# Kernel optimization log

Measured on AMD Instinct MI355X. Metric: run time of the kernel, lower is better.

Reference implementation:

```python
import jax, jax.numpy as jnp
import numpy as np

MU, SIGMA = -9.1232, 3.5412
FFT_SIZES = [8, 16, 32, 64]
HOP_SIZES = [2, 4, 8, 16]
EPS_MAG, EPS_SC = 1e-7, 1e-8


def hann_periodic(n):
    # torch.hann_window default (periodic=True)
    return 0.5 * (1.0 - jnp.cos(2.0 * jnp.pi * jnp.arange(n, dtype=jnp.float32) / n))


def stft_mag(xf, n_fft, hop):
    # xf: (rows, T). Matches torch.stft(center=True, pad_mode='reflect', onesided).
    pad = n_fft // 2
    xp = jnp.pad(xf, ((0, 0), (pad, pad)), mode='reflect')
    n_frames = 1 + (xp.shape[-1] - n_fft) // hop
    idx = jnp.arange(n_frames)[:, None] * hop + jnp.arange(n_fft)[None, :]
    frames = xp[:, idx] * hann_periodic(n_fft)  # (rows, n_frames, n_fft)
    spec = jnp.fft.rfft(frames, axis=-1)        # (rows, n_frames, n_fft//2+1)
    return jnp.abs(spec) + EPS_MAG


def setup_inputs() -> dict:
    key = jax.random.key(0)
    k1, k2 = jax.random.split(key)
    x = jax.random.normal(k1, (32, 1, 128, 1024), dtype=jnp.float32)
    y = jax.random.normal(k2, (32, 1, 128, 1024), dtype=jnp.float32)
    return {"x": x, "y": y}


def reference(x, y):
    B, C, F_mel, T = x.shape
    x_flat = jnp.exp(x * SIGMA + MU).reshape(-1, T)  # un-normalize log-mel -> linear
    y_flat = jnp.exp(y * SIGMA + MU).reshape(-1, T)
    loss_sc = jnp.float32(0.0)
    loss_mag = jnp.float32(0.0)
    for n_fft, hop in zip(FFT_SIZES, HOP_SIZES):
        x_mag = stft_mag(x_flat, n_fft, hop)
        y_mag = stft_mag(y_flat, n_fft, hop)
        sc = jnp.linalg.norm((y_mag - x_mag).ravel()) / (
            jnp.linalg.norm(y_mag.ravel()) + EPS_SC)
        mag = jnp.mean(jnp.abs(jnp.log(x_mag) - jnp.log(y_mag)))
        loss_sc = loss_sc + sc
        loss_mag = loss_mag + mag
    n = len(FFT_SIZES)
    return (loss_sc / n, loss_mag / n)
```

## Files before the change

### kernel.cpp

```cpp
#include <hip/hip_runtime.h>
#include <math.h>

static constexpr float kSigma = 3.5412f;
static constexpr float kMu    = -9.1232f;

constexpr double kPId = 3.14159265358979323846264338327950288;

constexpr double tp_sin(double r) {
    const double r2 = r * r;
    double t = r, s = r;
    t *= -r2 / (2.0 * 3.0);   s += t;
    t *= -r2 / (4.0 * 5.0);   s += t;
    t *= -r2 / (6.0 * 7.0);   s += t;
    t *= -r2 / (8.0 * 9.0);   s += t;
    t *= -r2 / (10.0 * 11.0); s += t;
    t *= -r2 / (12.0 * 13.0); s += t;
    return s;
}
constexpr double tp_cos(double r) {
    const double r2 = r * r;
    double t = 1.0, c = 1.0;
    t *= -r2 / (1.0 * 2.0);   c += t;
    t *= -r2 / (3.0 * 4.0);   c += t;
    t *= -r2 / (5.0 * 6.0);   c += t;
    t *= -r2 / (7.0 * 8.0);   c += t;
    t *= -r2 / (9.0 * 10.0);  c += t;
    t *= -r2 / (11.0 * 12.0); c += t;
    return c;
}
constexpr float ctw_c(int k, int n) {
    const int kk = ((k % n) + n) % n;
    const int q = (4 * kk) / n;
    const int num = 4 * kk - q * n;
    const double r = (2.0 * kPId * num) / (4.0 * n);
    const double cr = tp_cos(r), sr = tp_sin(r);
    return (float)(q == 0 ? cr : q == 1 ? -sr : q == 2 ? -cr : sr);
}
constexpr float ctw_ns(int k, int n) {
    const int kk = ((k % n) + n) % n;
    const int q = (4 * kk) / n;
    const int num = 4 * kk - q * n;
    const double r = (2.0 * kPId * num) / (4.0 * n);
    const double cr = tp_cos(r), sr = tp_sin(r);
    const double s = (q == 0 ? sr : q == 1 ? cr : q == 2 ? -sr : -cr);
    return (float)(-s);
}

__device__ __forceinline__ float pair_swap(float v) {
    return __int_as_float(__builtin_amdgcn_mov_dpp(__float_as_int(v), 0xB1, 0xF, 0xF, true));
}

#define DECLZ \
    float zr0=0.f,zi0=0.f, zr1=0.f,zi1=0.f, zr2=0.f,zi2=0.f, zr3=0.f,zi3=0.f, \
          zr4=0.f,zi4=0.f, zr5=0.f,zi5=0.f, zr6=0.f,zi6=0.f, zr7=0.f,zi7=0.f, \
          zr8=0.f,zi8=0.f, zr9=0.f,zi9=0.f, zr10=0.f,zi10=0.f, zr11=0.f,zi11=0.f; \
    (void)zr0;(void)zi0;(void)zr11;(void)zi11;

#define UPDB(n, m) \
    if constexpr ((n) >= 1 && (n) <= NB) { \
        constexpr int   k_ = (BSTART + (n) - 1) * ((m) + TAU * HH); \
        constexpr float c_ = ctw_c(k_, NN); \
        constexpr float s_ = ctw_ns(k_, NN); \
        zr##n = fmaf(d, c_, zr##n);  zi##n = fmaf(d, s_, zi##n); \
    }

#define ALLB(m) UPDB(1,m) UPDB(2,m) UPDB(3,m) UPDB(4,m) UPDB(5,m) \
                UPDB(6,m) UPDB(7,m) UPDB(8,m) UPDB(9,m) UPDB(10,m)

#define UPD_M(m) \
    if constexpr ((m) < HH) { \
        const float d = ps[off + TAU*HH + NN + (m)] - ps[off + TAU*HH + (m)]; \
        ALLB(m) \
        if constexpr (((m) & 7) == 7) __builtin_amdgcn_sched_barrier(0); \
    }
#define WRM_M(m) \
    if constexpr ((m) < HH) { \
        const float d = ps[TAU*HH + (m)]; \
        ALLB(m) \
        if constexpr (((m) & 7) == 7) __builtin_amdgcn_sched_barrier(0); \
    }

#define FORM(M) M(0) M(1) M(2) M(3) M(4) M(5) M(6) M(7) \
                M(8) M(9) M(10) M(11) M(12) M(13) M(14) M(15)

#define EMTB(nm, nc, np) \
    if constexpr (((nc) - 1) >= EJ0 && ((nc) - 1) < EJ0 + EN) { \
        constexpr int BG = BSTART + (nc) - 1; \
        float wr, wi; \
        if constexpr (BG == 0) { \
            const float s_ = (PH==0) ? zr##np : (PH==1) ? -zi##np : (PH==2) ? -zr##np : zi##np; \
            wr = 0.5f*zr##nc - 0.5f*s_;  wi = 0.5f*zi##nc; \
        } else if constexpr (BG == NN/2) { \
            const float s_ = (PH==0) ? zr##nm : (PH==1) ? zi##nm : (PH==2) ? -zr##nm : -zi##nm; \
            wr = 0.5f*zr##nc - 0.5f*s_;  wi = 0.5f*zi##nc; \
        } else { \
            const float tr = (PH==0) ? (zr##nm + zr##np) : (PH==1) ? (zi##nm - zi##np) \
                           : (PH==2) ? (-zr##nm - zr##np) : (zi##np - zi##nm); \
            const float ti = (PH==0) ? (zi##nm + zi##np) : (PH==1) ? (zr##np - zr##nm) \
                           : (PH==2) ? (-zi##nm - zi##np) : (zr##nm - zr##np); \
            wr = fmaf(-0.25f, tr, 0.5f*zr##nc);  wi = fmaf(-0.25f, ti, 0.5f*zi##nc); \
        } \
        const float pm   = fmaf(wr, wr, wi*wi); \
        const float mag  = sqrtf(pm) + 1e-7f; \
        const float lg   = __log2f(mag); \
        const float mago = pair_swap(mag); \
        const float lgo  = pair_swap(lg); \
        const float d_   = mag - mago; \
        sd2 = fmaf(d_, d_, sd2); \
        sy2 = fmaf(mag, mag, sy2); \
        slg += fabsf(lg - lgo); \
    }

#define FOREMT(M) M(0,1,2) M(1,2,3) M(2,3,4) M(3,4,5) M(4,5,6) \
                  M(5,6,7) M(6,7,8) M(7,8,9) M(8,9,10) M(9,10,11)

#define SLOT(t) { constexpr int TAU = (t); constexpr int PH = (t); FOREMT(EMTB) FORM(UPD_M) }
#define WARM(t) { constexpr int TAU = (t); FORM(WRM_M) }

template <int NN, int BSTART, int NB, int EJ0, int EN, int OFF, int LOG2SEGS>
__device__ __forceinline__ void run_group(const float* __restrict__ ps_,
                                          int seg, float& sd2, float& sy2, float& slg)
{
    constexpr int HH = NN / 4;
    constexpr int FF = 4096 / NN + 1;
    constexpr int NQ = FF >> (LOG2SEGS + 2);
    const int t0 = (seg * FF) >> LOG2SEGS;
    const int t1 = ((seg + 1) * FF) >> LOG2SEGS;
    const int L  = t1 - t0;
    const float* __restrict__ ps = ps_ + OFF + t0 * HH;

    DECLZ
    WARM(0) WARM(1) WARM(2) WARM(3)

    int off = 0;
#pragma unroll
    for (int q = 0; q < NQ; ++q) {
        SLOT(0) SLOT(1) SLOT(2) SLOT(3)
        off += 4 * HH;
    }
    if (L > 4 * NQ) { SLOT(0) }
}

template <int NN, int NGROUPS>
__global__ __launch_bounds__(256, 4)
void sdft_kernel(const float* __restrict__ xg, const float* __restrict__ yg,
                 float* __restrict__ acc )
{
    constexpr int RS = 1106;
    __shared__ float ldsx[4][RS];
    __shared__ float ldsy[4][RS];
    __shared__ float red[4][3];

    const int tid  = threadIdx.x;
    const int row0 = blockIdx.x << 2;

#pragma unroll 1
    for (int task = tid; task < 2048; task += 256) {
        const int q = task & 255, rr = (task >> 8) & 3, sg = task >> 10;
        const float* __restrict__ src = sg ? yg : xg;
        const float4 v = reinterpret_cast<const float4*>(src)[((row0 + rr) << 8) + q];
        float* dst = (sg ? &ldsy[rr][0] : &ldsx[rr][0]) + 32 + (q << 2);
        dst[0] = __expf(fmaf(v.x, kSigma, kMu));
        dst[1] = __expf(fmaf(v.y, kSigma, kMu));
        dst[2] = __expf(fmaf(v.z, kSigma, kMu));
        dst[3] = __expf(fmaf(v.w, kSigma, kMu));
    }
#pragma unroll 1
    for (int task = tid; task < 640; task += 256) {
        const int p = task % 80, rem_ = task / 80;
        const int rr = rem_ & 3, sg = rem_ >> 2;
        const int j = (p < 32) ? p : (1024 + p);
        float v = 0.f;
        if (j < 1088) {
            const int i = (j < 32) ? (32 - j) : (2078 - j);
            const float* __restrict__ src = sg ? yg : xg;
            v = __expf(fmaf(src[((row0 + rr) << 10) + i], kSigma, kMu));
        }
        (sg ? ldsy[rr] : ldsx[rr])[j] = v;
    }
    __syncthreads();

    constexpr int GL2 = (NGROUPS == 4) ? 2 : (NGROUPS == 2) ? 1 : 0;
    constexpr int LOG2SEGS = 5 - GL2;
    const int wid  = tid >> 6, lane = tid & 63;
    const int group  = wid & (NGROUPS - 1);
    const int segblk = wid >> GL2;
    const int seg  = (segblk << 3) | (lane >> 3);
    const int row  = (lane >> 1) & 3;
    const int sig  = lane & 1;
    const float* ps = sig ? &ldsy[row][0] : &ldsx[row][0];

    float sd2 = 0.f, sy2 = 0.f, slg = 0.f;
    if constexpr (NN == 64) {
        switch (group) {
            case 0:  run_group<64,  0,  9, 0, 8,  0, LOG2SEGS>(ps, seg, sd2, sy2, slg); break;
            case 1:  run_group<64,  7, 10, 1, 8,  0, LOG2SEGS>(ps, seg, sd2, sy2, slg); break;
            case 2:  run_group<64, 15, 10, 1, 8,  0, LOG2SEGS>(ps, seg, sd2, sy2, slg); break;
            default: run_group<64, 23, 10, 1, 9,  0, LOG2SEGS>(ps, seg, sd2, sy2, slg); break;
        }
    } else if constexpr (NN == 32) {
        if (group == 0) run_group<32,  0,  9, 0, 8, 16, LOG2SEGS>(ps, seg, sd2, sy2, slg);
        else            run_group<32,  7, 10, 1, 9, 16, LOG2SEGS>(ps, seg, sd2, sy2, slg);
    } else if constexpr (NN == 16) {
        run_group<16, 0, 9, 0, 9, 24, LOG2SEGS>(ps, seg, sd2, sy2, slg);
    } else {
        run_group< 8, 0, 5, 0, 5, 28, LOG2SEGS>(ps, seg, sd2, sy2, slg);
    }

    if (!sig) sy2 = 0.f;
#pragma unroll
    for (int o = 32; o > 0; o >>= 1) {
        sd2 += __shfl_down(sd2, o);
        sy2 += __shfl_down(sy2, o);
        slg += __shfl_down(slg, o);
    }
    if (lane == 0) { red[wid][0] = sd2; red[wid][1] = sy2; red[wid][2] = slg; }
    __syncthreads();
    if (tid == 0) {
        atomicAdd(&acc[0],   red[0][0] + red[1][0] + red[2][0] + red[3][0]);
        atomicAdd(&acc[64],  red[0][1] + red[1][1] + red[2][1] + red[3][1]);
        atomicAdd(&acc[128], red[0][2] + red[1][2] + red[2][2] + red[3][2]);
    }
}

__global__ void finalize_kernel(const float* __restrict__ acc, float* __restrict__ out)
{
    if (threadIdx.x == 0 && blockIdx.x == 0) {
        const float nel[4] = {10506240.f, 9474048.f, 8982528.f, 8785920.f};
        float sc = 0.f, mg = 0.f;
#pragma unroll
        for (int r = 0; r < 4; ++r) {
            const float a0 = acc[(r * 3 + 0) * 64];
            const float a1 = acc[(r * 3 + 1) * 64];
            const float a2 = acc[(r * 3 + 2) * 64];
            sc += sqrtf(a0 * 0.5f) / (sqrtf(a1) + 1e-8f);
            mg += a2 * 0.34657359028f / nel[r];
        }
        out[0] = sc * 0.25f;
        out[1] = mg * 0.25f;
    }
}

extern "C" void kernel_launch(void* const* d_in, const int* in_sizes, int n_in,
                              void* d_out, int out_size, void* d_ws, size_t ws_size,
                              hipStream_t stream)
{
    const float* x = (const float*)d_in[0];
    const float* y = (const float*)d_in[1];
    float* out = (float*)d_out;
    float* acc = (float*)d_ws;

    hipMemsetAsync(acc, 0, 12 * 64 * sizeof(float), stream);

    sdft_kernel<64, 4><<<1024, 256, 0, stream>>>(x, y, acc + 3 * 192);
    sdft_kernel<32, 2><<<1024, 256, 0, stream>>>(x, y, acc + 2 * 192);
    sdft_kernel<16, 1><<<1024, 256, 0, stream>>>(x, y, acc + 1 * 192);
    sdft_kernel< 8, 1><<<1024, 256, 0, stream>>>(x, y, acc + 0 * 192);

    finalize_kernel<<<1, 64, 0, stream>>>(acc, out);
}
```

Measured before the change: 144.2 us.

## Pad LDS rows with skew and per-kernel strides to remove bank conflicts

```diff
diff --git a/kernel.cpp b/kernel.cpp
--- a/kernel.cpp
+++ b/kernel.cpp
@@ -50,6 +50,8 @@
     return __int_as_float(__builtin_amdgcn_mov_dpp(__float_as_int(v), 0xB1, 0xF, 0xF, true));
 }
 
+#define KA(c) ((c) + ((c) >> 5))
+
 #define DECLZ \
     float zr0=0.f,zi0=0.f, zr1=0.f,zi1=0.f, zr2=0.f,zi2=0.f, zr3=0.f,zi3=0.f, \
           zr4=0.f,zi4=0.f, zr5=0.f,zi5=0.f, zr6=0.f,zi6=0.f, zr7=0.f,zi7=0.f, \
@@ -69,13 +71,13 @@
 
 #define UPD_M(m) \
     if constexpr ((m) < HH) { \
-        const float d = ps[off + TAU*HH + NN + (m)] - ps[off + TAU*HH + (m)]; \
+        const float d = psb[KA(QB + TAU*HH + NN + (m))] - psb[KA(QB + TAU*HH + (m))]; \
         ALLB(m) \
         if constexpr (((m) & 7) == 7) __builtin_amdgcn_sched_barrier(0); \
     }
 #define WRM_M(m) \
     if constexpr ((m) < HH) { \
-        const float d = ps[TAU*HH + (m)]; \
+        const float d = psb[KA(OFF + TAU*HH + (m))]; \
         ALLB(m) \
         if constexpr (((m) & 7) == 7) __builtin_amdgcn_sched_barrier(0); \
     }
@@ -114,31 +116,31 @@
 #define FOREMT(M) M(0,1,2) M(1,2,3) M(2,3,4) M(3,4,5) M(4,5,6) \
                   M(5,6,7) M(6,7,8) M(7,8,9) M(8,9,10) M(9,10,11)
 
-#define SLOT(t) { constexpr int TAU = (t); constexpr int PH = (t); FOREMT(EMTB) FORM(UPD_M) }
+#define SLOT(q, t) { constexpr int QB = OFF + 4*HH*(q); constexpr int TAU = (t); \
+                     constexpr int PH = (t); FOREMT(EMTB) FORM(UPD_M) }
+#define SLOT4(q) SLOT(q,0) SLOT(q,1) SLOT(q,2) SLOT(q,3)
 #define WARM(t) { constexpr int TAU = (t); FORM(WRM_M) }
 
 template <int NN, int BSTART, int NB, int EJ0, int EN, int OFF, int LOG2SEGS>
-__device__ __forceinline__ void run_group(const float* __restrict__ ps_,
+__device__ __forceinline__ void run_group(const float* __restrict__ ps0,
                                           int seg, float& sd2, float& sy2, float& slg)
 {
     constexpr int HH = NN / 4;
     constexpr int FF = 4096 / NN + 1;
     constexpr int NQ = FF >> (LOG2SEGS + 2);
+    static_assert(NQ == 2 || NQ == 4, "unroll pattern assumes NQ in {2,4}");
     const int t0 = (seg * FF) >> LOG2SEGS;
     const int t1 = ((seg + 1) * FF) >> LOG2SEGS;
     const int L  = t1 - t0;
-    const float* __restrict__ ps = ps_ + OFF + t0 * HH;
+    const int B  = t0 * HH;
+    const float* __restrict__ psb = ps0 + B + (B >> 5);
 
     DECLZ
     WARM(0) WARM(1) WARM(2) WARM(3)
 
-    int off = 0;
-#pragma unroll
-    for (int q = 0; q < NQ; ++q) {
-        SLOT(0) SLOT(1) SLOT(2) SLOT(3)
-        off += 4 * HH;
-    }
-    if (L > 4 * NQ) { SLOT(0) }
+    SLOT4(0) SLOT4(1)
+    if constexpr (NQ == 4) { SLOT4(2) SLOT4(3) }
+    if (L > 4 * NQ) { SLOT(NQ, 0) }
 }
 
 template <int NN, int NGROUPS>
@@ -146,9 +148,8 @@
 void sdft_kernel(const float* __restrict__ xg, const float* __restrict__ yg,
                  float* __restrict__ acc )
 {
-    constexpr int RS = 1106;
-    __shared__ float ldsx[4][RS];
-    __shared__ float ldsy[4][RS];
+    constexpr int RSTR = (NN == 64) ? 1153 : (NN == 32) ? 1161 : 1160;
+    __shared__ float lds[8][RSTR];
     __shared__ float red[4][3];
 
     const int tid  = threadIdx.x;
@@ -159,7 +160,8 @@
         const int q = task & 255, rr = (task >> 8) & 3, sg = task >> 10;
         const float* __restrict__ src = sg ? yg : xg;
         const float4 v = reinterpret_cast<const float4*>(src)[((row0 + rr) << 8) + q];
-        float* dst = (sg ? &ldsy[rr][0] : &ldsx[rr][0]) + 32 + (q << 2);
+        const int j = 32 + (q << 2);
+        float* dst = &lds[rr * 2 + sg][KA(j)];
         dst[0] = __expf(fmaf(v.x, kSigma, kMu));
         dst[1] = __expf(fmaf(v.y, kSigma, kMu));
         dst[2] = __expf(fmaf(v.z, kSigma, kMu));
@@ -176,7 +178,7 @@
             const float* __restrict__ src = sg ? yg : xg;
             v = __expf(fmaf(src[((row0 + rr) << 10) + i], kSigma, kMu));
         }
-        (sg ? ldsy[rr] : ldsx[rr])[j] = v;
+        lds[rr * 2 + sg][KA(j)] = v;
     }
     __syncthreads();
 
@@ -186,25 +188,24 @@
     const int group  = wid & (NGROUPS - 1);
     const int segblk = wid >> GL2;
     const int seg  = (segblk << 3) | (lane >> 3);
-    const int row  = (lane >> 1) & 3;
     const int sig  = lane & 1;
-    const float* ps = sig ? &ldsy[row][0] : &ldsx[row][0];
+    const float* ps0 = &lds[lane & 7][0];
 
     float sd2 = 0.f, sy2 = 0.f, slg = 0.f;
     if constexpr (NN == 64) {
         switch (group) {
-            case 0:  run_group<64,  0,  9, 0, 8,  0, LOG2SEGS>(ps, seg, sd2, sy2, slg); break;
-            case 1:  run_group<64,  7, 10, 1, 8,  0, LOG2SEGS>(ps, seg, sd2, sy2, slg); break;
-            case 2:  run_group<64, 15, 10, 1, 8,  0, LOG2SEGS>(ps, seg, sd2, sy2, slg); break;
-            default: run_group<64, 23, 10, 1, 9,  0, LOG2SEGS>(ps, seg, sd2, sy2, slg); break;
+            case 0:  run_group<64,  0,  9, 0, 8,  0, LOG2SEGS>(ps0, seg, sd2, sy2, slg); break;
+            case 1:  run_group<64,  7, 10, 1, 8,  0, LOG2SEGS>(ps0, seg, sd2, sy2, slg); break;
+            case 2:  run_group<64, 15, 10, 1, 8,  0, LOG2SEGS>(ps0, seg, sd2, sy2, slg); break;
+            default: run_group<64, 23, 10, 1, 9,  0, LOG2SEGS>(ps0, seg, sd2, sy2, slg); break;
         }
     } else if constexpr (NN == 32) {
-        if (group == 0) run_group<32,  0,  9, 0, 8, 16, LOG2SEGS>(ps, seg, sd2, sy2, slg);
-        else            run_group<32,  7, 10, 1, 9, 16, LOG2SEGS>(ps, seg, sd2, sy2, slg);
+        if (group == 0) run_group<32,  0,  9, 0, 8, 16, LOG2SEGS>(ps0, seg, sd2, sy2, slg);
+        else            run_group<32,  7, 10, 1, 9, 16, LOG2SEGS>(ps0, seg, sd2, sy2, slg);
     } else if constexpr (NN == 16) {
-        run_group<16, 0, 9, 0, 9, 24, LOG2SEGS>(ps, seg, sd2, sy2, slg);
+        run_group<16, 0, 9, 0, 9, 24, LOG2SEGS>(ps0, seg, sd2, sy2, slg);
     } else {
-        run_group< 8, 0, 5, 0, 5, 28, LOG2SEGS>(ps, seg, sd2, sy2, slg);
+        run_group< 8, 0, 5, 0, 5, 28, LOG2SEGS>(ps0, seg, sd2, sy2, slg);
     }
 
     if (!sig) sy2 = 0.f;
```

Measured after the change: 151.7 us. 5.2% more time.
